# Kernel tuning notes

Measured on AMD Instinct MI355X. Metric: run time of the kernel, lower is better.

Reference implementation:

```python
import jax, jax.numpy as jnp
import numpy as np

B = 16384          # batch rows
L = 50             # ids per row (constant row length)
NNZ = B * L        # total ragged values
NUM_BUCKETS = 8192


def setup_inputs() -> dict:
    key = jax.random.key(0)
    k1, k2 = jax.random.split(key)
    values = jax.random.randint(k1, (NNZ, 1), 0, NUM_BUCKETS, dtype=jnp.int32)
    row_lengths = jnp.full((B, 1), L, dtype=jnp.int32)
    weight_values = jax.random.uniform(k2, (NNZ, 1), dtype=jnp.float32)
    return {
        "values": values,
        "row_lengths": row_lengths,
        "weight_values": weight_values,
        "weight_row_lengths": row_lengths,
    }


def reference(values, row_lengths, weight_values, weight_row_lengths):
    # Math of safe_embedding_lookup_sparse against an identity table with
    # combiner='sum': out[b, id] += w for each (id, w) in row b.
    ids = values[:, 0]                     # [NNZ]
    w = weight_values[:, 0]                # [NNZ]
    nrows = row_lengths.shape[0]
    # Expand row_lengths to per-value row ids (ragged segment ids).
    row_ids = jnp.repeat(jnp.arange(nrows, dtype=jnp.int32),
                         row_lengths[:, 0],
                         total_repeat_length=ids.shape[0])  # [NNZ]
    out = jnp.zeros((nrows, NUM_BUCKETS), dtype=jnp.float32)
    out = out.at[row_ids, ids].add(w)      # weighted histogram scatter-add
    return out
```

## Files before the change

kernel.cpp:

```cpp
#include <hip/hip_runtime.h>
#include <hip/hip_bf16.h>

#define NUM_BUCKETS 8192
#define ROW_THREADS 256
#define SCAN_THREADS 1024

typedef float f32x4 __attribute__((ext_vector_type(4)));

__global__ __launch_bounds__(SCAN_THREADS) void scan_rows_kernel(
    const int* __restrict__ row_len, int* __restrict__ offs, int B) {
    __shared__ int buf[SCAN_THREADS];
    __shared__ int carry_s;
    const int t = threadIdx.x;
    if (t == 0) carry_s = 0;
    __syncthreads();
    for (int base = 0; base < B; base += SCAN_THREADS) {
        const int i = base + t;
        const int v = (i < B) ? row_len[i] : 0;
        buf[t] = v;
        __syncthreads();
        for (int off = 1; off < SCAN_THREADS; off <<= 1) {
            int add = (t >= off) ? buf[t - off] : 0;
            __syncthreads();
            buf[t] += add;
            __syncthreads();
        }
        const int carry = carry_s;
        __syncthreads();
        if (i < B) offs[i] = carry + buf[t] - v;
        if (t == SCAN_THREADS - 1) {
            carry_s = carry + buf[t];
            if (base + SCAN_THREADS >= B) offs[B] = carry + buf[t];
        }
        __syncthreads();
    }
}

__global__ __launch_bounds__(ROW_THREADS) void nhot_row_kernel(
    const int* __restrict__ ids, const float* __restrict__ w,
    const int* __restrict__ offs, float* __restrict__ out) {
    __shared__ float lds[NUM_BUCKETS];
    const int r = blockIdx.x;
    const int t = threadIdx.x;

    #pragma unroll
    for (int k = 0; k < NUM_BUCKETS / ROW_THREADS; ++k)
        lds[k * ROW_THREADS + t] = 0.0f;
    __syncthreads();

    const int s = offs[r];
    const int e = offs[r + 1];
    for (int i = s + t; i < e; i += ROW_THREADS) {
        atomicAdd(&lds[ids[i]], w[i]);
    }
    __syncthreads();

    f32x4* outv = reinterpret_cast<f32x4*>(out + (size_t)r * NUM_BUCKETS);
    const f32x4* ldsv = reinterpret_cast<const f32x4*>(lds);
    #pragma unroll
    for (int k = 0; k < NUM_BUCKETS / 4 / ROW_THREADS; ++k) {
        __builtin_nontemporal_store(ldsv[k * ROW_THREADS + t],
                                    &outv[k * ROW_THREADS + t]);
    }
}

extern "C" void kernel_launch(void* const* d_in, const int* in_sizes, int n_in,
                              void* d_out, int out_size, void* d_ws, size_t ws_size,
                              hipStream_t stream) {
    const int*   ids     = (const int*)d_in[0];
    const int*   row_len = (const int*)d_in[1];
    const float* wvals   = (const float*)d_in[2];

    const int B = in_sizes[1];
    float* out = (float*)d_out;
    int* offs = (int*)d_ws;

    scan_rows_kernel<<<1, SCAN_THREADS, 0, stream>>>(row_len, offs, B);
    nhot_row_kernel<<<B, ROW_THREADS, 0, stream>>>(ids, wvals, offs, out);
}
```

Measured before the change: 132.2 us.

## Replace LDS Hillis-Steele scan with wave-shuffle scan and vectorize LDS zeroing

Rewrites the single-block row-length prefix scan: each thread now serially scans 16 elements, then wave-level shuffle scans and a small cross-wave scan combine the results. The old version did a barrier-heavy shared-memory Hillis-Steele scan over 16 chunks of 1024. The change also zeroes the shared histogram with 128-bit vector stores instead of scalar stores. The per-thread strided loads of 16 consecutive ints are uncoalesced, but the input is only 64KB.

```diff
diff --git a/kernel.cpp b/kernel.cpp
--- a/kernel.cpp
+++ b/kernel.cpp
@@ -3,35 +3,58 @@
 
 #define NUM_BUCKETS 8192
 #define ROW_THREADS 256
-#define SCAN_THREADS 1024
 
 typedef float f32x4 __attribute__((ext_vector_type(4)));
 
-__global__ __launch_bounds__(SCAN_THREADS) void scan_rows_kernel(
+__global__ __launch_bounds__(1024) void scan_rows_kernel(
     const int* __restrict__ row_len, int* __restrict__ offs, int B) {
-    __shared__ int buf[SCAN_THREADS];
+    __shared__ int wave_sums[16];
     __shared__ int carry_s;
     const int t = threadIdx.x;
+    const int wave = t >> 6, lane = t & 63;
     if (t == 0) carry_s = 0;
     __syncthreads();
-    for (int base = 0; base < B; base += SCAN_THREADS) {
-        const int i = base + t;
-        const int v = (i < B) ? row_len[i] : 0;
-        buf[t] = v;
+    const int CHUNK = 1024 * 16;
+    for (int base = 0; base < B; base += CHUNK) {
+        int v[16];
+        const int idx0 = base + t * 16;
+        int local = 0;
+        #pragma unroll
+        for (int e = 0; e < 16; ++e) {
+            const int i = idx0 + e;
+            const int x = (i < B) ? row_len[i] : 0;
+            v[e] = local;
+            local += x;
+        }
+        int incl = local;
+        #pragma unroll
+        for (int d = 1; d < 64; d <<= 1) {
+            const int y = __shfl_up(incl, d, 64);
+            if (lane >= d) incl += y;
+        }
+        if (lane == 63) wave_sums[wave] = incl;
         __syncthreads();
-        for (int off = 1; off < SCAN_THREADS; off <<= 1) {
-            int add = (t >= off) ? buf[t - off] : 0;
-            __syncthreads();
-            buf[t] += add;
-            __syncthreads();
+        if (wave == 0) {
+            int s = (lane < 16) ? wave_sums[lane] : 0;
+            #pragma unroll
+            for (int d = 1; d < 16; d <<= 1) {
+                const int y = __shfl_up(s, d, 64);
+                if (lane >= d) s += y;
+            }
+            if (lane < 16) wave_sums[lane] = s;
         }
+        __syncthreads();
         const int carry = carry_s;
+        const int wave_excl = (wave == 0) ? 0 : wave_sums[wave - 1];
+        const int texcl = carry + wave_excl + (incl - local);
+        #pragma unroll
+        for (int e = 0; e < 16; ++e) {
+            const int i = idx0 + e;
+            if (i < B) offs[i] = texcl + v[e];
+        }
+        if (t == 0 && base + CHUNK >= B) offs[B] = carry + wave_sums[15];
         __syncthreads();
-        if (i < B) offs[i] = carry + buf[t] - v;
-        if (t == SCAN_THREADS - 1) {
-            carry_s = carry + buf[t];
-            if (base + SCAN_THREADS >= B) offs[B] = carry + buf[t];
-        }
+        if (t == 0) carry_s = carry + wave_sums[15];
         __syncthreads();
     }
 }
@@ -43,9 +66,11 @@
     const int r = blockIdx.x;
     const int t = threadIdx.x;
 
+    f32x4* ldsv = reinterpret_cast<f32x4*>(lds);
+    const f32x4 z = {0.f, 0.f, 0.f, 0.f};
     #pragma unroll
-    for (int k = 0; k < NUM_BUCKETS / ROW_THREADS; ++k)
-        lds[k * ROW_THREADS + t] = 0.0f;
+    for (int k = 0; k < NUM_BUCKETS / 4 / ROW_THREADS; ++k)
+        ldsv[k * ROW_THREADS + t] = z;
     __syncthreads();
 
     const int s = offs[r];
@@ -56,7 +81,6 @@
     __syncthreads();
 
     f32x4* outv = reinterpret_cast<f32x4*>(out + (size_t)r * NUM_BUCKETS);
-    const f32x4* ldsv = reinterpret_cast<const f32x4*>(lds);
     #pragma unroll
     for (int k = 0; k < NUM_BUCKETS / 4 / ROW_THREADS; ++k) {
         __builtin_nontemporal_store(ldsv[k * ROW_THREADS + t],
@@ -75,6 +99,6 @@
     float* out = (float*)d_out;
     int* offs = (int*)d_ws;
 
-    scan_rows_kernel<<<1, SCAN_THREADS, 0, stream>>>(row_len, offs, B);
+    scan_rows_kernel<<<1, 1024, 0, stream>>>(row_len, offs, B);
     nhot_row_kernel<<<B, ROW_THREADS, 0, stream>>>(ids, wvals, offs, out);
 }
```

After: 118.3 us. 10.6% less time.
